# Performance work log

Hardware: AMD Instinct MI355X
Metric: run time of the kernel (lower is better)

## Reference

```python
import jax, jax.numpy as jnp
import numpy as np

N = 100000
E = 1600000
IN_DIM = 128
OUT_DIM = 128
H = 4
HD = OUT_DIM // H  # 32
NEG_SLOPE = 0.2
EPS_SOFTMAX = 1e-8
EPS_LN = 1e-5


def setup_inputs() -> dict:
    key = jax.random.key(0)
    ks = jax.random.split(key, 6)
    h = jax.random.normal(ks[0], (N, IN_DIM), dtype=jnp.float32)
    edge_index = jax.random.randint(ks[1], (2, E), 0, N, dtype=jnp.int32)
    W = jax.random.normal(ks[2], (IN_DIM, OUT_DIM), dtype=jnp.float32) / np.sqrt(IN_DIM)
    W_self = jax.random.normal(ks[3], (IN_DIM, OUT_DIM), dtype=jnp.float32) / np.sqrt(IN_DIM)
    a_in = jax.random.normal(ks[4], (H, 2 * HD), dtype=jnp.float32) * 0.01
    a_out = jax.random.normal(ks[5], (H, 2 * HD), dtype=jnp.float32) * 0.01
    bias = jnp.zeros((OUT_DIM,), dtype=jnp.float32)
    ln_gamma = jnp.ones((OUT_DIM,), dtype=jnp.float32)
    ln_beta = jnp.zeros((OUT_DIM,), dtype=jnp.float32)
    return {"h": h, "edge_index": edge_index, "W": W, "W_self": W_self,
            "a_in": a_in, "a_out": a_out, "bias": bias,
            "ln_gamma": ln_gamma, "ln_beta": ln_beta}


def _attention_aggregate(h_proj, sender, receiver, attn_vec, num_nodes):
    # h_proj: (N, H, HD); sender/receiver: (E,); attn_vec: (H, 2*HD)
    h_sender = h_proj[sender]      # (E, H, HD)
    h_receiver = h_proj[receiver]  # (E, H, HD)
    # e = sum over concat([h_sender, h_receiver]) * attn_vec, split halves
    e = (jnp.einsum('ehd,hd->eh', h_sender, attn_vec[:, :HD])
         + jnp.einsum('ehd,hd->eh', h_receiver, attn_vec[:, HD:]))
    e = jax.nn.leaky_relu(e, NEG_SLOPE)
    e_max = jax.ops.segment_max(e, receiver, num_segments=num_nodes)  # (N, H)
    alpha = jnp.exp(e - e_max[receiver])
    alpha_sum = jax.ops.segment_sum(alpha, receiver, num_segments=num_nodes)
    alpha = alpha / (alpha_sum[receiver] + EPS_SOFTMAX)
    msg = h_sender * alpha[..., None]  # (E, H, HD)
    return jax.ops.segment_sum(msg, receiver, num_segments=num_nodes)  # (N, H, HD)


def reference(h, edge_index, W, W_self, a_in, a_out, bias, ln_gamma, ln_beta):
    n = h.shape[0]
    h_proj = (h @ W).reshape(n, H, HD)
    h_self = h @ W_self
    src, dst = edge_index[0], edge_index[1]
    h_in = _attention_aggregate(h_proj, src, dst, a_in, n)   # 'in' direction
    h_out = _attention_aggregate(h_proj, dst, src, a_out, n)  # 'out' direction
    combined = h_self + h_in.reshape(n, -1) + h_out.reshape(n, -1) + bias
    mean = combined.mean(axis=-1, keepdims=True)
    var = combined.var(axis=-1, keepdims=True)
    normed = (combined - mean) * jax.lax.rsqrt(var + EPS_LN)
    return normed * ln_gamma + ln_beta
```

## Files before the change

### kernel.cpp

```cpp
#include <hip/hip_runtime.h>
#include <math.h>

#define HEADS 4
#define HD 32
#define DIM 128
#define NEG_SLOPE 0.2f
#define EPS_SM 1e-8f
#define EPS_LN 1e-5f
#define SH1 9
#define PB 128
#define BCOLS 272

typedef _Float16 h2_t __attribute__((ext_vector_type(2)));
typedef _Float16 f16x8 __attribute__((ext_vector_type(8)));
typedef float f32x4 __attribute__((ext_vector_type(4)));

__device__ __forceinline__ float lrelu(float x) { return x > 0.f ? x : NEG_SLOPE * x; }
__device__ __forceinline__ unsigned pkh(float a, float b) {
    return __builtin_bit_cast(unsigned, __builtin_amdgcn_cvt_pkrtz(a, b));
}
__device__ __forceinline__ float dot2(unsigned a, unsigned b, float c) {
    return __builtin_amdgcn_fdot2(__builtin_bit_cast(h2_t, a), __builtin_bit_cast(h2_t, b), c, false);
}

template<int LIM> __device__ __forceinline__ void rmax4(float& a, float& b, float& c, float& d) {
#pragma unroll
    for (int s = 1; s < LIM; s <<= 1) {
        a = fmaxf(a, __shfl_xor(a, s, 64));
        b = fmaxf(b, __shfl_xor(b, s, 64));
        c = fmaxf(c, __shfl_xor(c, s, 64));
        d = fmaxf(d, __shfl_xor(d, s, 64));
    }
}
template<int LIM> __device__ __forceinline__ void rsum4(float& a, float& b, float& c, float& d) {
#pragma unroll
    for (int s = 1; s < LIM; s <<= 1) {
        a += __shfl_xor(a, s, 64);
        b += __shfl_xor(b, s, 64);
        c += __shfl_xor(c, s, 64);
        d += __shfl_xor(d, s, 64);
    }
}

__global__ __launch_bounds__(128) void cvtb_k(const float* __restrict__ W,
                                              const float* __restrict__ V,
                                              const float* __restrict__ a_in,
                                              const float* __restrict__ a_out,
                                              _Float16* __restrict__ Bt) {
    const int c = blockIdx.x;
    const int k = threadIdx.x;
    float v;
    if (c < 128) {
        v = W[k * 128 + c];
    } else if (c < 256) {
        v = V[k * 128 + (c - 128)];
    } else {
        int d = (c - 256) >> 2, h = (c - 256) & 3;
        const float* a = (d < 2) ? a_in : a_out;
        int base = h * 64 + (d & 1) * 32;
        float s = 0.f;
#pragma unroll
        for (int t = 0; t < 32; ++t) s += W[k * 128 + 32 * h + t] * a[base + t];
        v = s;
    }
    Bt[c * 128 + k] = (_Float16)v;
}

__global__ __launch_bounds__(256) void mfma_gemm_k(const float* __restrict__ h,
                                                   const _Float16* __restrict__ Bt,
                                                   float* __restrict__ h_self,
                                                   unsigned* __restrict__ hp_pk,
                                                   float* __restrict__ pA0, float* __restrict__ pA1,
                                                   float* __restrict__ pB0, float* __restrict__ pB1,
                                                   int N) {
    __shared__ _Float16 hs[64][128];
    const int tid = threadIdx.x;
    const int w = tid >> 6, l = tid & 63;
    const int l15 = l & 15;
    const int kg = l >> 4;
    const int row0 = blockIdx.x * 64;
    const int arow = row0 + 16 * w + l15;

    f32x4 acc[17];
#pragma unroll
    for (int j = 0; j < 17; ++j) {
        acc[j][0] = 0.f; acc[j][1] = 0.f; acc[j][2] = 0.f; acc[j][3] = 0.f;
    }

    const uint4* __restrict__ bt4 = (const uint4*)Bt;

#pragma unroll
    for (int kc = 0; kc < 4; ++kc) {
        union { unsigned u[4]; f16x8 v; } cv;
        if (arow < N) {
            float4 x0 = ((const float4*)h)[(size_t)arow * 32 + kc * 8 + kg * 2];
            float4 x1 = ((const float4*)h)[(size_t)arow * 32 + kc * 8 + kg * 2 + 1];
            cv.u[0] = pkh(x0.x, x0.y); cv.u[1] = pkh(x0.z, x0.w);
            cv.u[2] = pkh(x1.x, x1.y); cv.u[3] = pkh(x1.z, x1.w);
        } else {
            cv.u[0] = 0u; cv.u[1] = 0u; cv.u[2] = 0u; cv.u[3] = 0u;
        }
        f16x8 af = cv.v;
#pragma unroll
        for (int j = 0; j < 17; ++j) {
            int col = 16 * j + l15;
            union { uint4 q; f16x8 v; } bc;
            bc.q = bt4[col * 16 + kc * 4 + kg];
            acc[j] = __builtin_amdgcn_mfma_f32_16x16x32_f16(af, bc.v, acc[j], 0, 0, 0);
        }
    }

    const int r4 = kg * 4;
    const int c16 = l15, dsel = c16 >> 2, hh = c16 & 3;
    float* __restrict__ pd = (dsel == 0) ? pA0 : (dsel == 1) ? pA1 : (dsel == 2) ? pB0 : pB1;
#pragma unroll
    for (int r = 0; r < 4; ++r) {
        int grow = row0 + 16 * w + r4 + r;
        bool ok = grow < N;
#pragma unroll
        for (int j = 8; j < 16; ++j)
            if (ok) h_self[(size_t)grow * 128 + 16 * (j - 8) + l15] = acc[j][r];
        if (ok) pd[grow * 4 + hh] = acc[16][r];
#pragma unroll
        for (int j = 0; j < 8; ++j)
            hs[16 * w + r4 + r][16 * j + l15] = (_Float16)acc[j][r];
    }
    __syncthreads();
    const uint4* hsv = (const uint4*)&hs[0][0];
#pragma unroll
    for (int p = 0; p < 4; ++p) {
        int chunk = tid + p * 256;
        int rrow = chunk >> 4, cg = chunk & 15;
        int grow = row0 + rrow;
        if (grow < N)
            ((uint4*)hp_pk)[(size_t)grow * 16 + cg] = hsv[rrow * 16 + cg];
    }
}

__global__ __launch_bounds__(256) void part1a_k(const int* __restrict__ ei, int* __restrict__ cntmat,
                                                int E, int N, int NBIN) {
    __shared__ int lcnt[512];
    const int t = threadIdx.x;
    const int CH = (E + gridDim.x - 1) / gridDim.x;
    const int e0 = blockIdx.x * CH;
    const int e1 = min(e0 + CH, E);
    for (int i = t; i < 512; i += 256) lcnt[i] = 0;
    __syncthreads();
    for (int e = e0 + t; e < e1; e += 256) {
        int s = ei[e], d = ei[E + e];
        atomicAdd(&lcnt[d >> SH1], 1);
        atomicAdd(&lcnt[(N + s) >> SH1], 1);
    }
    __syncthreads();
    for (int i = t; i < NBIN; i += 256) cntmat[i * PB + blockIdx.x] = lcnt[i];
}

__global__ __launch_bounds__(128) void scanB_k(const int* __restrict__ cntmat,
                                               int* __restrict__ blkoff, int* __restrict__ btot) {
    __shared__ int ls[PB];
    const int bin = blockIdx.x;
    const int t = threadIdx.x;
    int v = cntmat[bin * PB + t];
    ls[t] = v;
    __syncthreads();
#pragma unroll
    for (int d = 1; d < PB; d <<= 1) {
        int u = (t >= d) ? ls[t - d] : 0;
        __syncthreads();
        ls[t] += u;
        __syncthreads();
    }
    blkoff[bin * PB + t] = ls[t] - v;
    if (t == PB - 1) btot[bin] = ls[t];
}

__global__ __launch_bounds__(256) void scanC_k(const int* __restrict__ btot,
                                               int* __restrict__ bbase, int NBIN, int twoE) {
    __shared__ int ls[256];
    int t = threadIdx.x;
    int i0 = 2 * t, i1 = 2 * t + 1;
    int v0 = (i0 < NBIN) ? btot[i0] : 0;
    int v1 = (i1 < NBIN) ? btot[i1] : 0;
    int pair = v0 + v1;
    ls[t] = pair;
    __syncthreads();
#pragma unroll
    for (int d = 1; d < 256; d <<= 1) {
        int u = (t >= d) ? ls[t - d] : 0;
        __syncthreads();
        ls[t] += u;
        __syncthreads();
    }
    int excl = ls[t] - pair;
    if (i0 < NBIN) bbase[i0] = excl;
    if (i1 < NBIN) bbase[i1] = excl + v0;
    if (t == 0) bbase[NBIN] = twoE;
}

__global__ __launch_bounds__(256) void part1b_k(const int* __restrict__ ei,
                                                const int* __restrict__ bbase,
                                                const int* __restrict__ blkoff,
                                                unsigned* __restrict__ rec, int E, int N, int NBIN) {
    __shared__ int gb[512];
    __shared__ int lcur[512];
    const int t = threadIdx.x;
    const int CH = (E + gridDim.x - 1) / gridDim.x;
    const int e0 = blockIdx.x * CH;
    const int e1 = min(e0 + CH, E);
    for (int i = t; i < 512; i += 256) lcur[i] = 0;
    for (int i = t; i < NBIN; i += 256) gb[i] = bbase[i] + blkoff[i * PB + blockIdx.x];
    __syncthreads();
    for (int e = e0 + t; e < e1; e += 256) {
        int s = ei[e], d = ei[E + e];
        int b1 = d >> SH1;
        int r1 = atomicAdd(&lcur[b1], 1);
        rec[gb[b1] + r1] = (unsigned)s | ((unsigned)(d & 511) << 20);
        int so = N + s;
        int b2 = so >> SH1;
        int r2 = atomicAdd(&lcur[b2], 1);
        rec[gb[b2] + r2] = (unsigned)d | ((unsigned)(so & 511) << 20);
    }
}

__global__ __launch_bounds__(256) void build2_k(const unsigned* __restrict__ rec,
                                                const int* __restrict__ bbase,
                                                int* __restrict__ off, int* __restrict__ csr,
                                                int M, int twoE, int NBIN) {
    __shared__ int lcnt[512];
    __shared__ int lcur[512];
    __shared__ int ls[256];
    const int b = blockIdx.x;
    const int t = threadIdx.x;
    const int base = bbase[b];
    const int cnt = bbase[b + 1] - base;
    const int seg0 = b << SH1;
    for (int i = t; i < 512; i += 256) lcnt[i] = 0;
    __syncthreads();
    for (int k = t; k < cnt; k += 256) atomicAdd(&lcnt[rec[base + k] >> 20], 1);
    __syncthreads();
    int v0 = lcnt[2 * t], v1 = lcnt[2 * t + 1];
    int pair = v0 + v1;
    ls[t] = pair;
    __syncthreads();
#pragma unroll
    for (int d = 1; d < 256; d <<= 1) {
        int u = (t >= d) ? ls[t - d] : 0;
        __syncthreads();
        ls[t] += u;
        __syncthreads();
    }
    int excl = ls[t] - pair;
    lcur[2 * t] = excl;
    lcur[2 * t + 1] = excl + v0;
    int sg = seg0 + 2 * t;
    if (sg < M) off[sg] = base + excl;
    if (sg + 1 < M) off[sg + 1] = base + excl + v0;
    if (b == NBIN - 1 && t == 0) off[M] = twoE;
    __syncthreads();
    for (int k = t; k < cnt; k += 256) {
        unsigned r = rec[base + k];
        int pos = atomicAdd(&lcur[r >> 20], 1);
        csr[base + pos] = (int)(r & 0xFFFFFu);
    }
}

__global__ __launch_bounds__(256) void node_aggr_ln_k(const unsigned* __restrict__ hp_pk,
                                                      const float* __restrict__ h_self,
                                                      const float* __restrict__ pA0, const float* __restrict__ pA1,
                                                      const float* __restrict__ pB0, const float* __restrict__ pB1,
                                                      const int* __restrict__ off, const int* __restrict__ csr,
                                                      const float* __restrict__ bias,
                                                      const float* __restrict__ gamma,
                                                      const float* __restrict__ beta,
                                                      float* __restrict__ out, int N) {
    __shared__ int sds[4][64];
    __shared__ uint2 wts[4][64];
    const int wave = threadIdx.x >> 6;
    const int lane = threadIdx.x & 63;
    const int n = blockIdx.x * 4 + wave;
    if (n >= N) return;
    const int l15 = lane & 15;
    const int q = lane >> 4;
    const unsigned wsel = (l15 & 4) ? 0x07060302u : 0x05040100u;
    const bool hlo = (l15 < 8);
    int* sdw = sds[wave];
    uint2* wtw = wts[wave];
    const char* hpb = (const char*)hp_pk;
    const unsigned rowoff = (unsigned)l15 << 4;

    float acc[8];
#pragma unroll
    for (int k = 0; k < 8; ++k) acc[k] = 0.f;

#pragma unroll
    for (int dir = 0; dir < 2; ++dir) {
        const int seg = (dir == 0) ? n : N + n;
        const int beg = off[seg], end = off[seg + 1];
        const int len = end - beg;
        if (len == 0) continue;
        const float* __restrict__ p0 = (dir == 0) ? pA0 : pB0;
        const float* __restrict__ p1 = (dir == 0) ? pA1 : pB1;
        float4 r1 = ((const float4*)p1)[n];

        if (len <= 64) {
            int sid = 0;
            float e0 = -INFINITY, e1 = -INFINITY, e2 = -INFINITY, e3 = -INFINITY;
            if (lane < len) {
                sid = csr[beg + lane];
                float4 r0 = ((const float4*)p0)[sid];
                e0 = lrelu(r0.x + r1.x);
                e1 = lrelu(r0.y + r1.y);
                e2 = lrelu(r0.z + r1.z);
                e3 = lrelu(r0.w + r1.w);
            }
            float m0 = e0, m1 = e1, m2 = e2, m3 = e3;
            if (len <= 16)      rmax4<16>(m0, m1, m2, m3);
            else if (len <= 32) rmax4<32>(m0, m1, m2, m3);
            else                rmax4<64>(m0, m1, m2, m3);
            float w0 = 0.f, w1 = 0.f, w2 = 0.f, w3 = 0.f;
            if (lane < len) {
                w0 = __expf(e0 - m0); w1 = __expf(e1 - m1);
                w2 = __expf(e2 - m2); w3 = __expf(e3 - m3);
            }
            float s0 = w0, s1 = w1, s2 = w2, s3 = w3;
            if (len <= 16)      rsum4<16>(s0, s1, s2, s3);
            else if (len <= 32) rsum4<32>(s0, s1, s2, s3);
            else                rsum4<64>(s0, s1, s2, s3);
            w0 *= 1.f / (s0 + EPS_SM);
            w1 *= 1.f / (s1 + EPS_SM);
            w2 *= 1.f / (s2 + EPS_SM);
            w3 *= 1.f / (s3 + EPS_SM);
            sdw[lane] = sid;
            wtw[lane] = make_uint2(pkh(w0, w1), pkh(w2, w3));
            const int npair = (len + 7) >> 3;
#pragma unroll 2
            for (int t = 0; t < npair; ++t) {
                int pi = 4 * t + q;
                uint2 sp = *(const uint2*)&sdw[2 * pi];
                uint4 wp = *(const uint4*)&wtw[2 * pi];
                uint4 u = *(const uint4*)(hpb + (((unsigned)sp.x << 8) + rowoff));
                uint4 v = *(const uint4*)(hpb + (((unsigned)sp.y << 8) + rowoff));
                unsigned wA = hlo ? wp.x : wp.y;
                unsigned wB = hlo ? wp.z : wp.w;
                unsigned wpk = __builtin_amdgcn_perm(wB, wA, wsel);
                acc[0] = dot2(__builtin_amdgcn_perm(v.x, u.x, 0x05040100u), wpk, acc[0]);
                acc[1] = dot2(__builtin_amdgcn_perm(v.x, u.x, 0x07060302u), wpk, acc[1]);
                acc[2] = dot2(__builtin_amdgcn_perm(v.y, u.y, 0x05040100u), wpk, acc[2]);
                acc[3] = dot2(__builtin_amdgcn_perm(v.y, u.y, 0x07060302u), wpk, acc[3]);
                acc[4] = dot2(__builtin_amdgcn_perm(v.z, u.z, 0x05040100u), wpk, acc[4]);
                acc[5] = dot2(__builtin_amdgcn_perm(v.z, u.z, 0x07060302u), wpk, acc[5]);
                acc[6] = dot2(__builtin_amdgcn_perm(v.w, u.w, 0x05040100u), wpk, acc[6]);
                acc[7] = dot2(__builtin_amdgcn_perm(v.w, u.w, 0x07060302u), wpk, acc[7]);
            }
        } else {
            float m0 = -INFINITY, m1 = -INFINITY, m2 = -INFINITY, m3 = -INFINITY;
            for (int base = beg; base < end; base += 64) {
                int j = base + lane;
                if (j < end) {
                    int sid = csr[j];
                    float4 r0 = ((const float4*)p0)[sid];
                    m0 = fmaxf(m0, lrelu(r0.x + r1.x));
                    m1 = fmaxf(m1, lrelu(r0.y + r1.y));
                    m2 = fmaxf(m2, lrelu(r0.z + r1.z));
                    m3 = fmaxf(m3, lrelu(r0.w + r1.w));
                }
            }
            rmax4<64>(m0, m1, m2, m3);
            float s0 = 0.f, s1 = 0.f, s2 = 0.f, s3 = 0.f;
            for (int base = beg; base < end; base += 64) {
                int j = base + lane;
                if (j < end) {
                    int sid = csr[j];
                    float4 r0 = ((const float4*)p0)[sid];
                    s0 += __expf(lrelu(r0.x + r1.x) - m0);
                    s1 += __expf(lrelu(r0.y + r1.y) - m1);
                    s2 += __expf(lrelu(r0.z + r1.z) - m2);
                    s3 += __expf(lrelu(r0.w + r1.w) - m3);
                }
            }
            rsum4<64>(s0, s1, s2, s3);
            const float is0 = 1.f / (s0 + EPS_SM);
            const float is1 = 1.f / (s1 + EPS_SM);
            const float is2 = 1.f / (s2 + EPS_SM);
            const float is3 = 1.f / (s3 + EPS_SM);
            for (int base = beg; base < end; base += 64) {
                int cnt = min(64, end - base);
                int sid = 0;
                float w0 = 0.f, w1 = 0.f, w2 = 0.f, w3 = 0.f;
                if (lane < cnt) {
                    sid = csr[base + lane];
                    float4 r0 = ((const float4*)p0)[sid];
                    w0 = __expf(lrelu(r0.x + r1.x) - m0) * is0;
                    w1 = __expf(lrelu(r0.y + r1.y) - m1) * is1;
                    w2 = __expf(lrelu(r0.z + r1.z) - m2) * is2;
                    w3 = __expf(lrelu(r0.w + r1.w) - m3) * is3;
                }
                sdw[lane] = sid;
                wtw[lane] = make_uint2(pkh(w0, w1), pkh(w2, w3));
                const int npair = (cnt + 7) >> 3;
#pragma unroll 2
                for (int t = 0; t < npair; ++t) {
                    int pi = 4 * t + q;
                    uint2 sp = *(const uint2*)&sdw[2 * pi];
                    uint4 wp = *(const uint4*)&wtw[2 * pi];
                    uint4 u = *(const uint4*)(hpb + (((unsigned)sp.x << 8) + rowoff));
                    uint4 v = *(const uint4*)(hpb + (((unsigned)sp.y << 8) + rowoff));
                    unsigned wA = hlo ? wp.x : wp.y;
                    unsigned wB = hlo ? wp.z : wp.w;
                    unsigned wpk = __builtin_amdgcn_perm(wB, wA, wsel);
                    acc[0] = dot2(__builtin_amdgcn_perm(v.x, u.x, 0x05040100u), wpk, acc[0]);
                    acc[1] = dot2(__builtin_amdgcn_perm(v.x, u.x, 0x07060302u), wpk, acc[1]);
                    acc[2] = dot2(__builtin_amdgcn_perm(v.y, u.y, 0x05040100u), wpk, acc[2]);
                    acc[3] = dot2(__builtin_amdgcn_perm(v.y, u.y, 0x07060302u), wpk, acc[3]);
                    acc[4] = dot2(__builtin_amdgcn_perm(v.z, u.z, 0x05040100u), wpk, acc[4]);
                    acc[5] = dot2(__builtin_amdgcn_perm(v.z, u.z, 0x07060302u), wpk, acc[5]);
                    acc[6] = dot2(__builtin_amdgcn_perm(v.w, u.w, 0x05040100u), wpk, acc[6]);
                    acc[7] = dot2(__builtin_amdgcn_perm(v.w, u.w, 0x07060302u), wpk, acc[7]);
                }
            }
        }
    }

#pragma unroll
    for (int s = 16; s < 64; s <<= 1) {
#pragma unroll
        for (int k = 0; k < 8; ++k) acc[k] += __shfl_xor(acc[k], s, 64);
    }

    size_t bb = (size_t)n * DIM;
    float4 hs0 = ((const float4*)(h_self + bb))[2 * l15];
    float4 hs1 = ((const float4*)(h_self + bb))[2 * l15 + 1];
    float4 b0 = ((const float4*)bias)[2 * l15];
    float4 b1 = ((const float4*)bias)[2 * l15 + 1];
    float x0 = hs0.x + acc[0] + b0.x;
    float x1 = hs0.y + acc[1] + b0.y;
    float x2 = hs0.z + acc[2] + b0.z;
    float x3 = hs0.w + acc[3] + b0.w;
    float y0 = hs1.x + acc[4] + b1.x;
    float y1 = hs1.y + acc[5] + b1.y;
    float y2 = hs1.z + acc[6] + b1.z;
    float y3 = hs1.w + acc[7] + b1.w;
    float sum = x0 + x1 + x2 + x3 + y0 + y1 + y2 + y3;
    float sq = x0 * x0 + x1 * x1 + x2 * x2 + x3 * x3
             + y0 * y0 + y1 * y1 + y2 * y2 + y3 * y3;
#pragma unroll
    for (int m = 1; m < 64; m <<= 1) {
        sum += __shfl_xor(sum, m, 64);
        sq += __shfl_xor(sq, m, 64);
    }
    float mean = sum * (1.f / 512.f);
    float var = sq * (1.f / 512.f) - mean * mean;
    float inv = rsqrtf(var + EPS_LN);
    if (lane < 16) {
        float4 g0 = ((const float4*)gamma)[2 * l15];
        float4 g1 = ((const float4*)gamma)[2 * l15 + 1];
        float4 be0 = ((const float4*)beta)[2 * l15];
        float4 be1 = ((const float4*)beta)[2 * l15 + 1];
        float4 o0 = make_float4((x0 - mean) * inv * g0.x + be0.x,
                                (x1 - mean) * inv * g0.y + be0.y,
                                (x2 - mean) * inv * g0.z + be0.z,
                                (x3 - mean) * inv * g0.w + be0.w);
        float4 o1 = make_float4((y0 - mean) * inv * g1.x + be1.x,
                                (y1 - mean) * inv * g1.y + be1.y,
                                (y2 - mean) * inv * g1.z + be1.z,
                                (y3 - mean) * inv * g1.w + be1.w);
        ((float4*)(out + bb))[2 * l15] = o0;
        ((float4*)(out + bb))[2 * l15 + 1] = o1;
    }
}

extern "C" void kernel_launch(void* const* d_in, const int* in_sizes, int n_in,
                              void* d_out, int out_size, void* d_ws, size_t ws_size,
                              hipStream_t stream) {
    const float* h      = (const float*)d_in[0];
    const int*   ei     = (const int*)d_in[1];
    const float* W      = (const float*)d_in[2];
    const float* W_self = (const float*)d_in[3];
    const float* a_in   = (const float*)d_in[4];
    const float* a_out  = (const float*)d_in[5];
    const float* bias   = (const float*)d_in[6];
    const float* gamma  = (const float*)d_in[7];
    const float* beta   = (const float*)d_in[8];
    float* out = (float*)d_out;

    const int N = in_sizes[0] / DIM;
    const int E = in_sizes[1] / 2;
    const int M = 2 * N;
    const int NBIN = (M + (1 << SH1) - 1) >> SH1;
    const int twoE = 2 * E;

    float* ws = (float*)d_ws;
    size_t off_f = 0;
    float* h_self = ws + off_f; off_f += (size_t)N * DIM;
    unsigned* hp_pk = (unsigned*)(ws + off_f); off_f += (size_t)N * 64;
    float* pA0 = ws + off_f; off_f += (size_t)N * 4;
    float* pA1 = ws + off_f; off_f += (size_t)N * 4;
    float* pB0 = ws + off_f; off_f += (size_t)N * 4;
    float* pB1 = ws + off_f; off_f += (size_t)N * 4;
    int* ip = (int*)(ws + off_f);
    size_t off_i = 0;
    int* cntmat = ip + off_i; off_i += (size_t)NBIN * PB;
    int* blkoff = ip + off_i; off_i += (size_t)NBIN * PB;
    int* btot   = ip + off_i; off_i += NBIN;
    int* bbase  = ip + off_i; off_i += (size_t)NBIN + 1;
    int* off    = ip + off_i; off_i += (size_t)M + 1;
    unsigned* rec = (unsigned*)(ip + off_i); off_i += (size_t)twoE;
    int* csr    = ip + off_i; off_i += (size_t)twoE;
    _Float16* Bt = (_Float16*)(ip + off_i); off_i += (size_t)(BCOLS * 128) / 2;

    cvtb_k<<<BCOLS, 128, 0, stream>>>(W, W_self, a_in, a_out, Bt);

    part1a_k<<<PB, 256, 0, stream>>>(ei, cntmat, E, N, NBIN);
    scanB_k<<<NBIN, PB, 0, stream>>>(cntmat, blkoff, btot);
    scanC_k<<<1, 256, 0, stream>>>(btot, bbase, NBIN, twoE);
    part1b_k<<<PB, 256, 0, stream>>>(ei, bbase, blkoff, rec, E, N, NBIN);
    build2_k<<<NBIN, 256, 0, stream>>>(rec, bbase, off, csr, M, twoE, NBIN);

    mfma_gemm_k<<<(N + 63) / 64, 256, 0, stream>>>(h, Bt, h_self, hp_pk,
                                                   pA0, pA1, pB0, pB1, N);

    node_aggr_ln_k<<<(N + 3) / 4, 256, 0, stream>>>(hp_pk, h_self, pA0, pA1, pB0, pB1,
                                                    off, csr, bias, gamma, beta, out, N);
}
```

Baseline: 417.1 us.

## Fuse weight prep into count kernel, store h_self in fp16, merge both directions

Folds the weight-conversion kernel into the edge-count kernel as extra blocks, removing one launch. Stores the self-projection h_self as packed fp16 instead of fp32, halving its write and read traffic. Processes both edge directions in one pass over the wave when each degree is at most 32, with each half-wave handling one direction and a shared aggregation loop. The fp16 h_self costs some precision in the residual term.

```diff
diff --git a/kernel.cpp b/kernel.cpp
--- a/kernel.cpp
+++ b/kernel.cpp
@@ -22,6 +22,8 @@
 __device__ __forceinline__ float dot2(unsigned a, unsigned b, float c) {
     return __builtin_amdgcn_fdot2(__builtin_bit_cast(h2_t, a), __builtin_bit_cast(h2_t, b), c, false);
 }
+__device__ __forceinline__ float lo16(unsigned u) { return (float)__builtin_bit_cast(h2_t, u)[0]; }
+__device__ __forceinline__ float hi16(unsigned u) { return (float)__builtin_bit_cast(h2_t, u)[1]; }
 
 template<int LIM> __device__ __forceinline__ void rmax4(float& a, float& b, float& c, float& d) {
 #pragma unroll
@@ -42,38 +44,85 @@
     }
 }
 
-__global__ __launch_bounds__(128) void cvtb_k(const float* __restrict__ W,
-                                              const float* __restrict__ V,
-                                              const float* __restrict__ a_in,
-                                              const float* __restrict__ a_out,
-                                              _Float16* __restrict__ Bt) {
-    const int c = blockIdx.x;
-    const int k = threadIdx.x;
-    float v;
-    if (c < 128) {
-        v = W[k * 128 + c];
-    } else if (c < 256) {
-        v = V[k * 128 + (c - 128)];
-    } else {
-        int d = (c - 256) >> 2, h = (c - 256) & 3;
-        const float* a = (d < 2) ? a_in : a_out;
-        int base = h * 64 + (d & 1) * 32;
-        float s = 0.f;
-#pragma unroll
-        for (int t = 0; t < 32; ++t) s += W[k * 128 + 32 * h + t] * a[base + t];
-        v = s;
-    }
-    Bt[c * 128 + k] = (_Float16)v;
+__device__ __forceinline__ void aggr_pairs(int cnt, const int* __restrict__ sdw,
+                                           const uint2* __restrict__ wtw,
+                                           const char* __restrict__ hpb,
+                                           unsigned rowoff, int q, bool hlo, unsigned wsel,
+                                           float (&acc)[8]) {
+    const int npair = (cnt + 7) >> 3;
+#pragma unroll 2
+    for (int t = 0; t < npair; ++t) {
+        int pi = 4 * t + q;
+        uint2 sp = *(const uint2*)&sdw[2 * pi];
+        uint4 wp = *(const uint4*)&wtw[2 * pi];
+        uint4 u = *(const uint4*)(hpb + (((unsigned)sp.x << 8) + rowoff));
+        uint4 v = *(const uint4*)(hpb + (((unsigned)sp.y << 8) + rowoff));
+        unsigned wA = hlo ? wp.x : wp.y;
+        unsigned wB = hlo ? wp.z : wp.w;
+        unsigned wpk = __builtin_amdgcn_perm(wB, wA, wsel);
+        acc[0] = dot2(__builtin_amdgcn_perm(v.x, u.x, 0x05040100u), wpk, acc[0]);
+        acc[1] = dot2(__builtin_amdgcn_perm(v.x, u.x, 0x07060302u), wpk, acc[1]);
+        acc[2] = dot2(__builtin_amdgcn_perm(v.y, u.y, 0x05040100u), wpk, acc[2]);
+        acc[3] = dot2(__builtin_amdgcn_perm(v.y, u.y, 0x07060302u), wpk, acc[3]);
+        acc[4] = dot2(__builtin_amdgcn_perm(v.z, u.z, 0x05040100u), wpk, acc[4]);
+        acc[5] = dot2(__builtin_amdgcn_perm(v.z, u.z, 0x07060302u), wpk, acc[5]);
+        acc[6] = dot2(__builtin_amdgcn_perm(v.w, u.w, 0x05040100u), wpk, acc[6]);
+        acc[7] = dot2(__builtin_amdgcn_perm(v.w, u.w, 0x07060302u), wpk, acc[7]);
+    }
+}
+
+__global__ __launch_bounds__(256) void part1a_k(const int* __restrict__ ei, int* __restrict__ cntmat,
+                                                int E, int N, int NBIN,
+                                                const float* __restrict__ W,
+                                                const float* __restrict__ V,
+                                                const float* __restrict__ a_in,
+                                                const float* __restrict__ a_out,
+                                                _Float16* __restrict__ Bt) {
+    __shared__ int lcnt[512];
+    const int t = threadIdx.x;
+    if (blockIdx.x >= PB) {
+        int c = (blockIdx.x - PB) * 2 + (t >> 7);
+        int k = t & 127;
+        float v;
+        if (c < 128) {
+            v = W[k * 128 + c];
+        } else if (c < 256) {
+            v = V[k * 128 + (c - 128)];
+        } else {
+            int d = (c - 256) >> 2, hh = (c - 256) & 3;
+            const float* a = (d < 2) ? a_in : a_out;
+            int base = hh * 64 + (d & 1) * 32;
+            float s = 0.f;
+#pragma unroll
+            for (int tt = 0; tt < 32; ++tt) s += W[k * 128 + 32 * hh + tt] * a[base + tt];
+            v = s;
+        }
+        Bt[c * 128 + k] = (_Float16)v;
+        return;
+    }
+    const int CH = (E + PB - 1) / PB;
+    const int e0 = blockIdx.x * CH;
+    const int e1 = min(e0 + CH, E);
+    for (int i = t; i < 512; i += 256) lcnt[i] = 0;
+    __syncthreads();
+    for (int e = e0 + t; e < e1; e += 256) {
+        int s = ei[e], d = ei[E + e];
+        atomicAdd(&lcnt[d >> SH1], 1);
+        atomicAdd(&lcnt[(N + s) >> SH1], 1);
+    }
+    __syncthreads();
+    for (int i = t; i < NBIN; i += 256) cntmat[i * PB + blockIdx.x] = lcnt[i];
 }
 
 __global__ __launch_bounds__(256) void mfma_gemm_k(const float* __restrict__ h,
                                                    const _Float16* __restrict__ Bt,
-                                                   float* __restrict__ h_self,
+                                                   unsigned* __restrict__ hs_pk,
                                                    unsigned* __restrict__ hp_pk,
                                                    float* __restrict__ pA0, float* __restrict__ pA1,
                                                    float* __restrict__ pB0, float* __restrict__ pB1,
                                                    int N) {
     __shared__ _Float16 hs[64][128];
+    __shared__ _Float16 hss[64][128];
     const int tid = threadIdx.x;
     const int w = tid >> 6, l = tid & 63;
     const int l15 = l & 15;
@@ -111,48 +160,33 @@
     }
 
     const int r4 = kg * 4;
-    const int c16 = l15, dsel = c16 >> 2, hh = c16 & 3;
+    const int dsel = l15 >> 2, hh = l15 & 3;
     float* __restrict__ pd = (dsel == 0) ? pA0 : (dsel == 1) ? pA1 : (dsel == 2) ? pB0 : pB1;
 #pragma unroll
     for (int r = 0; r < 4; ++r) {
-        int grow = row0 + 16 * w + r4 + r;
-        bool ok = grow < N;
+        int lr = 16 * w + r4 + r;
+        int grow = row0 + lr;
+#pragma unroll
+        for (int j = 0; j < 8; ++j)
+            hs[lr][16 * j + l15] = (_Float16)acc[j][r];
 #pragma unroll
         for (int j = 8; j < 16; ++j)
-            if (ok) h_self[(size_t)grow * 128 + 16 * (j - 8) + l15] = acc[j][r];
-        if (ok) pd[grow * 4 + hh] = acc[16][r];
-#pragma unroll
-        for (int j = 0; j < 8; ++j)
-            hs[16 * w + r4 + r][16 * j + l15] = (_Float16)acc[j][r];
+            hss[lr][16 * (j - 8) + l15] = (_Float16)acc[j][r];
+        if (grow < N) pd[grow * 4 + hh] = acc[16][r];
     }
     __syncthreads();
     const uint4* hsv = (const uint4*)&hs[0][0];
+    const uint4* hssv = (const uint4*)&hss[0][0];
 #pragma unroll
     for (int p = 0; p < 4; ++p) {
         int chunk = tid + p * 256;
         int rrow = chunk >> 4, cg = chunk & 15;
         int grow = row0 + rrow;
-        if (grow < N)
+        if (grow < N) {
             ((uint4*)hp_pk)[(size_t)grow * 16 + cg] = hsv[rrow * 16 + cg];
-    }
-}
-
-__global__ __launch_bounds__(256) void part1a_k(const int* __restrict__ ei, int* __restrict__ cntmat,
-                                                int E, int N, int NBIN) {
-    __shared__ int lcnt[512];
-    const int t = threadIdx.x;
-    const int CH = (E + gridDim.x - 1) / gridDim.x;
-    const int e0 = blockIdx.x * CH;
-    const int e1 = min(e0 + CH, E);
-    for (int i = t; i < 512; i += 256) lcnt[i] = 0;
-    __syncthreads();
-    for (int e = e0 + t; e < e1; e += 256) {
-        int s = ei[e], d = ei[E + e];
-        atomicAdd(&lcnt[d >> SH1], 1);
-        atomicAdd(&lcnt[(N + s) >> SH1], 1);
-    }
-    __syncthreads();
-    for (int i = t; i < NBIN; i += 256) cntmat[i * PB + blockIdx.x] = lcnt[i];
+            ((uint4*)hs_pk)[(size_t)grow * 16 + cg] = hssv[rrow * 16 + cg];
+        }
+    }
 }
 
 __global__ __launch_bounds__(128) void scanB_k(const int* __restrict__ cntmat,
@@ -265,7 +299,7 @@
 }
 
 __global__ __launch_bounds__(256) void node_aggr_ln_k(const unsigned* __restrict__ hp_pk,
-                                                      const float* __restrict__ h_self,
+                                                      const unsigned* __restrict__ hs_pk,
                                                       const float* __restrict__ pA0, const float* __restrict__ pA1,
                                                       const float* __restrict__ pB0, const float* __restrict__ pB1,
                                                       const int* __restrict__ off, const int* __restrict__ csr,
@@ -292,132 +326,138 @@
 #pragma unroll
     for (int k = 0; k < 8; ++k) acc[k] = 0.f;
 
-#pragma unroll
-    for (int dir = 0; dir < 2; ++dir) {
-        const int seg = (dir == 0) ? n : N + n;
-        const int beg = off[seg], end = off[seg + 1];
-        const int len = end - beg;
-        if (len == 0) continue;
-        const float* __restrict__ p0 = (dir == 0) ? pA0 : pB0;
-        const float* __restrict__ p1 = (dir == 0) ? pA1 : pB1;
-        float4 r1 = ((const float4*)p1)[n];
-
-        if (len <= 64) {
-            int sid = 0;
-            float e0 = -INFINITY, e1 = -INFINITY, e2 = -INFINITY, e3 = -INFINITY;
-            if (lane < len) {
-                sid = csr[beg + lane];
-                float4 r0 = ((const float4*)p0)[sid];
-                e0 = lrelu(r0.x + r1.x);
-                e1 = lrelu(r0.y + r1.y);
-                e2 = lrelu(r0.z + r1.z);
-                e3 = lrelu(r0.w + r1.w);
-            }
-            float m0 = e0, m1 = e1, m2 = e2, m3 = e3;
-            if (len <= 16)      rmax4<16>(m0, m1, m2, m3);
-            else if (len <= 32) rmax4<32>(m0, m1, m2, m3);
-            else                rmax4<64>(m0, m1, m2, m3);
-            float w0 = 0.f, w1 = 0.f, w2 = 0.f, w3 = 0.f;
-            if (lane < len) {
-                w0 = __expf(e0 - m0); w1 = __expf(e1 - m1);
-                w2 = __expf(e2 - m2); w3 = __expf(e3 - m3);
-            }
-            float s0 = w0, s1 = w1, s2 = w2, s3 = w3;
-            if (len <= 16)      rsum4<16>(s0, s1, s2, s3);
-            else if (len <= 32) rsum4<32>(s0, s1, s2, s3);
-            else                rsum4<64>(s0, s1, s2, s3);
-            w0 *= 1.f / (s0 + EPS_SM);
-            w1 *= 1.f / (s1 + EPS_SM);
-            w2 *= 1.f / (s2 + EPS_SM);
-            w3 *= 1.f / (s3 + EPS_SM);
-            sdw[lane] = sid;
-            wtw[lane] = make_uint2(pkh(w0, w1), pkh(w2, w3));
-            const int npair = (len + 7) >> 3;
-#pragma unroll 2
-            for (int t = 0; t < npair; ++t) {
-                int pi = 4 * t + q;
-                uint2 sp = *(const uint2*)&sdw[2 * pi];
-                uint4 wp = *(const uint4*)&wtw[2 * pi];
-                uint4 u = *(const uint4*)(hpb + (((unsigned)sp.x << 8) + rowoff));
-                uint4 v = *(const uint4*)(hpb + (((unsigned)sp.y << 8) + rowoff));
-                unsigned wA = hlo ? wp.x : wp.y;
-                unsigned wB = hlo ? wp.z : wp.w;
-                unsigned wpk = __builtin_amdgcn_perm(wB, wA, wsel);
-                acc[0] = dot2(__builtin_amdgcn_perm(v.x, u.x, 0x05040100u), wpk, acc[0]);
-                acc[1] = dot2(__builtin_amdgcn_perm(v.x, u.x, 0x07060302u), wpk, acc[1]);
-                acc[2] = dot2(__builtin_amdgcn_perm(v.y, u.y, 0x05040100u), wpk, acc[2]);
-                acc[3] = dot2(__builtin_amdgcn_perm(v.y, u.y, 0x07060302u), wpk, acc[3]);
-                acc[4] = dot2(__builtin_amdgcn_perm(v.z, u.z, 0x05040100u), wpk, acc[4]);
-                acc[5] = dot2(__builtin_amdgcn_perm(v.z, u.z, 0x07060302u), wpk, acc[5]);
-                acc[6] = dot2(__builtin_amdgcn_perm(v.w, u.w, 0x05040100u), wpk, acc[6]);
-                acc[7] = dot2(__builtin_amdgcn_perm(v.w, u.w, 0x07060302u), wpk, acc[7]);
-            }
-        } else {
-            float m0 = -INFINITY, m1 = -INFINITY, m2 = -INFINITY, m3 = -INFINITY;
-            for (int base = beg; base < end; base += 64) {
-                int j = base + lane;
-                if (j < end) {
-                    int sid = csr[j];
+    const int beg0 = off[n], end0 = off[n + 1];
+    const int beg1 = off[N + n], end1 = off[N + n + 1];
+    const int len0 = end0 - beg0, len1 = end1 - beg1;
+
+    if (len0 <= 32 && len1 <= 32) {
+        const int half = lane >> 5;
+        const int hl = lane & 31;
+        const int beg = half ? beg1 : beg0;
+        const int len = half ? len1 : len0;
+        const float* __restrict__ pp0 = half ? pB0 : pA0;
+        const float* __restrict__ pp1 = half ? pB1 : pA1;
+        float4 r1 = ((const float4*)pp1)[n];
+        int sid = 0;
+        float e0 = -INFINITY, e1 = -INFINITY, e2 = -INFINITY, e3 = -INFINITY;
+        if (hl < len) {
+            sid = csr[beg + hl];
+            float4 r0 = ((const float4*)pp0)[sid];
+            e0 = lrelu(r0.x + r1.x);
+            e1 = lrelu(r0.y + r1.y);
+            e2 = lrelu(r0.z + r1.z);
+            e3 = lrelu(r0.w + r1.w);
+        }
+        float m0 = e0, m1 = e1, m2 = e2, m3 = e3;
+        const bool small16 = (len0 <= 16 && len1 <= 16);
+        if (small16) rmax4<16>(m0, m1, m2, m3);
+        else         rmax4<32>(m0, m1, m2, m3);
+        float w0 = 0.f, w1 = 0.f, w2 = 0.f, w3 = 0.f;
+        if (hl < len) {
+            w0 = __expf(e0 - m0); w1 = __expf(e1 - m1);
+            w2 = __expf(e2 - m2); w3 = __expf(e3 - m3);
+        }
+        float s0 = w0, s1 = w1, s2 = w2, s3 = w3;
+        if (small16) rsum4<16>(s0, s1, s2, s3);
+        else         rsum4<32>(s0, s1, s2, s3);
+        w0 *= 1.f / (s0 + EPS_SM);
+        w1 *= 1.f / (s1 + EPS_SM);
+        w2 *= 1.f / (s2 + EPS_SM);
+        w3 *= 1.f / (s3 + EPS_SM);
+        sdw[lane] = 0;
+        wtw[lane] = make_uint2(0u, 0u);
+        if (hl < len) {
+            int pos = half ? len0 + hl : hl;
+            sdw[pos] = sid;
+            wtw[pos] = make_uint2(pkh(w0, w1), pkh(w2, w3));
+        }
+        aggr_pairs(len0 + len1, sdw, wtw, hpb, rowoff, q, hlo, wsel, acc);
+    } else {
+#pragma unroll
+        for (int dir = 0; dir < 2; ++dir) {
+            const int beg = (dir == 0) ? beg0 : beg1;
+            const int end = (dir == 0) ? end0 : end1;
+            const int len = end - beg;
+            if (len == 0) continue;
+            const float* __restrict__ p0 = (dir == 0) ? pA0 : pB0;
+            const float* __restrict__ p1 = (dir == 0) ? pA1 : pB1;
+            float4 r1 = ((const float4*)p1)[n];
+
+            if (len <= 64) {
+                int sid = 0;
+                float e0 = -INFINITY, e1 = -INFINITY, e2 = -INFINITY, e3 = -INFINITY;
+                if (lane < len) {
+                    sid = csr[beg + lane];
                     float4 r0 = ((const float4*)p0)[sid];
-                    m0 = fmaxf(m0, lrelu(r0.x + r1.x));
-                    m1 = fmaxf(m1, lrelu(r0.y + r1.y));
-                    m2 = fmaxf(m2, lrelu(r0.z + r1.z));
-                    m3 = fmaxf(m3, lrelu(r0.w + r1.w));
+                    e0 = lrelu(r0.x + r1.x);
+                    e1 = lrelu(r0.y + r1.y);
+                    e2 = lrelu(r0.z + r1.z);
+                    e3 = lrelu(r0.w + r1.w);
+                }
+                float m0 = e0, m1 = e1, m2 = e2, m3 = e3;
+                rmax4<64>(m0, m1, m2, m3);
+                float w0 = 0.f, w1 = 0.f, w2 = 0.f, w3 = 0.f;
+                if (lane < len) {
+                    w0 = __expf(e0 - m0); w1 = __expf(e1 - m1);
+                    w2 = __expf(e2 - m2); w3 = __expf(e3 - m3);
+                }
+                float s0 = w0, s1 = w1, s2 = w2, s3 = w3;
+                rsum4<64>(s0, s1, s2, s3);
+                w0 *= 1.f / (s0 + EPS_SM);
+                w1 *= 1.f / (s1 + EPS_SM);
+                w2 *= 1.f / (s2 + EPS_SM);
+                w3 *= 1.f / (s3 + EPS_SM);
+                sdw[lane] = sid;
+                wtw[lane] = make_uint2(pkh(w0, w1), pkh(w2, w3));
+                aggr_pairs(len, sdw, wtw, hpb, rowoff, q, hlo, wsel, acc);
+            } else {
+                float m0 = -INFINITY, m1 = -INFINITY, m2 = -INFINITY, m3 = -INFINITY;
+                for (int base = beg; base < end; base += 64) {
+                    int j = base + lane;
+                    if (j < end) {
+                        int sid = csr[j];
+                        float4 r0 = ((const float4*)p0)[sid];
+                        m0 = fmaxf(m0, lrelu(r0.x + r1.x));
+                        m1 = fmaxf(m1, lrelu(r0.y + r1.y));
+                        m2 = fmaxf(m2, lrelu(r0.z + r1.z));
+                        m3 = fmaxf(m3, lrelu(r0.w + r1.w));
+                    }
+                }
+                rmax4<64>(m0, m1, m2, m3);
+                float s0 = 0.f, s1 = 0.f, s2 = 0.f, s3 = 0.f;
+                for (int base = beg; base < end; base += 64) {
+                    int j = base + lane;
+                    if (j < end) {
+                        int sid = csr[j];
+                        float4 r0 = ((const float4*)p0)[sid];
+                        s0 += __expf(lrelu(r0.x + r1.x) - m0);
+                        s1 += __expf(lrelu(r0.y + r1.y) - m1);
+                        s2 += __expf(lrelu(r0.z + r1.z) - m2);
+                        s3 += __expf(lrelu(r0.w + r1.w) - m3);
+                    }
+                }
+                rsum4<64>(s0, s1, s2, s3);
+                const float is0 = 1.f / (s0 + EPS_SM);
+                const float is1 = 1.f / (s1 + EPS_SM);
+                const float is2 = 1.f / (s2 + EPS_SM);
+                const float is3 = 1.f / (s3 + EPS_SM);
+                for (int base = beg; base < end; base += 64) {
+                    int cnt = min(64, end - base);
+                    int sid = 0;
+                    float w0 = 0.f, w1 = 0.f, w2 = 0.f, w3 = 0.f;
+                    if (lane < cnt) {
+                        sid = csr[base + lane];
+                        float4 r0 = ((const float4*)p0)[sid];
+                        w0 = __expf(lrelu(r0.x + r1.x) - m0) * is0;
+                        w1 = __expf(lrelu(r0.y + r1.y) - m1) * is1;
+                        w2 = __expf(lrelu(r0.z + r1.z) - m2) * is2;
+                        w3 = __expf(lrelu(r0.w + r1.w) - m3) * is3;
+                    }
+                    sdw[lane] = sid;
+                    wtw[lane] = make_uint2(pkh(w0, w1), pkh(w2, w3));
+                    aggr_pairs(cnt, sdw, wtw, hpb, rowoff, q, hlo, wsel, acc);
                 }
             }
-            rmax4<64>(m0, m1, m2, m3);
-            float s0 = 0.f, s1 = 0.f, s2 = 0.f, s3 = 0.f;
-            for (int base = beg; base < end; base += 64) {
-                int j = base + lane;
-                if (j < end) {
-                    int sid = csr[j];
-                    float4 r0 = ((const float4*)p0)[sid];
-                    s0 += __expf(lrelu(r0.x + r1.x) - m0);
-                    s1 += __expf(lrelu(r0.y + r1.y) - m1);
-                    s2 += __expf(lrelu(r0.z + r1.z) - m2);
-                    s3 += __expf(lrelu(r0.w + r1.w) - m3);
-                }
-            }
-            rsum4<64>(s0, s1, s2, s3);
-            const float is0 = 1.f / (s0 + EPS_SM);
-            const float is1 = 1.f / (s1 + EPS_SM);
-            const float is2 = 1.f / (s2 + EPS_SM);
-            const float is3 = 1.f / (s3 + EPS_SM);
-            for (int base = beg; base < end; base += 64) {
-                int cnt = min(64, end - base);
-                int sid = 0;
-                float w0 = 0.f, w1 = 0.f, w2 = 0.f, w3 = 0.f;
-                if (lane < cnt) {
-                    sid = csr[base + lane];
-                    float4 r0 = ((const float4*)p0)[sid];
-                    w0 = __expf(lrelu(r0.x + r1.x) - m0) * is0;
-                    w1 = __expf(lrelu(r0.y + r1.y) - m1) * is1;
-                    w2 = __expf(lrelu(r0.z + r1.z) - m2) * is2;
-                    w3 = __expf(lrelu(r0.w + r1.w) - m3) * is3;
-                }
-                sdw[lane] = sid;
-                wtw[lane] = make_uint2(pkh(w0, w1), pkh(w2, w3));
-                const int npair = (cnt + 7) >> 3;
-#pragma unroll 2
-                for (int t = 0; t < npair; ++t) {
-                    int pi = 4 * t + q;
-                    uint2 sp = *(const uint2*)&sdw[2 * pi];
-                    uint4 wp = *(const uint4*)&wtw[2 * pi];
-                    uint4 u = *(const uint4*)(hpb + (((unsigned)sp.x << 8) + rowoff));
-                    uint4 v = *(const uint4*)(hpb + (((unsigned)sp.y << 8) + rowoff));
-                    unsigned wA = hlo ? wp.x : wp.y;
-                    unsigned wB = hlo ? wp.z : wp.w;
-                    unsigned wpk = __builtin_amdgcn_perm(wB, wA, wsel);
-                    acc[0] = dot2(__builtin_amdgcn_perm(v.x, u.x, 0x05040100u), wpk, acc[0]);
-                    acc[1] = dot2(__builtin_amdgcn_perm(v.x, u.x, 0x07060302u), wpk, acc[1]);
-                    acc[2] = dot2(__builtin_amdgcn_perm(v.y, u.y, 0x05040100u), wpk, acc[2]);
-                    acc[3] = dot2(__builtin_amdgcn_perm(v.y, u.y, 0x07060302u), wpk, acc[3]);
-                    acc[4] = dot2(__builtin_amdgcn_perm(v.z, u.z, 0x05040100u), wpk, acc[4]);
-                    acc[5] = dot2(__builtin_amdgcn_perm(v.z, u.z, 0x07060302u), wpk, acc[5]);
-                    acc[6] = dot2(__builtin_amdgcn_perm(v.w, u.w, 0x05040100u), wpk, acc[6]);
-                    acc[7] = dot2(__builtin_amdgcn_perm(v.w, u.w, 0x07060302u), wpk, acc[7]);
-                }
-            }
         }
     }
 
@@ -428,18 +468,17 @@
     }
 
     size_t bb = (size_t)n * DIM;
-    float4 hs0 = ((const float4*)(h_self + bb))[2 * l15];
-    float4 hs1 = ((const float4*)(h_self + bb))[2 * l15 + 1];
+    uint4 hv = ((const uint4*)hs_pk)[(size_t)n * 16 + l15];
     float4 b0 = ((const float4*)bias)[2 * l15];
     float4 b1 = ((const float4*)bias)[2 * l15 + 1];
-    float x0 = hs0.x + acc[0] + b0.x;
-    float x1 = hs0.y + acc[1] + b0.y;
-    float x2 = hs0.z + acc[2] + b0.z;
-    float x3 = hs0.w + acc[3] + b0.w;
-    float y0 = hs1.x + acc[4] + b1.x;
-    float y1 = hs1.y + acc[5] + b1.y;
-    float y2 = hs1.z + acc[6] + b1.z;
-    float y3 = hs1.w + acc[7] + b1.w;
+    float x0 = lo16(hv.x) + acc[0] + b0.x;
+    float x1 = hi16(hv.x) + acc[1] + b0.y;
+    float x2 = lo16(hv.y) + acc[2] + b0.z;
+    float x3 = hi16(hv.y) + acc[3] + b0.w;
+    float y0 = lo16(hv.z) + acc[4] + b1.x;
+    float y1 = hi16(hv.z) + acc[5] + b1.y;
+    float y2 = lo16(hv.w) + acc[6] + b1.z;
+    float y3 = hi16(hv.w) + acc[7] + b1.w;
     float sum = x0 + x1 + x2 + x3 + y0 + y1 + y2 + y3;
     float sq = x0 * x0 + x1 * x1 + x2 * x2 + x3 * x3
              + y0 * y0 + y1 * y1 + y2 * y2 + y3 * y3;
@@ -491,7 +530,7 @@
 
     float* ws = (float*)d_ws;
     size_t off_f = 0;
-    float* h_self = ws + off_f; off_f += (size_t)N * DIM;
+    unsigned* hs_pk = (unsigned*)(ws + off_f); off_f += (size_t)N * 64;
     unsigned* hp_pk = (unsigned*)(ws + off_f); off_f += (size_t)N * 64;
     float* pA0 = ws + off_f; off_f += (size_t)N * 4;
     float* pA1 = ws + off_f; off_f += (size_t)N * 4;
@@ -508,17 +547,16 @@
     int* csr    = ip + off_i; off_i += (size_t)twoE;
     _Float16* Bt = (_Float16*)(ip + off_i); off_i += (size_t)(BCOLS * 128) / 2;
 
-    cvtb_k<<<BCOLS, 128, 0, stream>>>(W, W_self, a_in, a_out, Bt);
-
-    part1a_k<<<PB, 256, 0, stream>>>(ei, cntmat, E, N, NBIN);
+    part1a_k<<<PB + BCOLS / 2, 256, 0, stream>>>(ei, cntmat, E, N, NBIN,
+                                                 W, W_self, a_in, a_out, Bt);
     scanB_k<<<NBIN, PB, 0, stream>>>(cntmat, blkoff, btot);
     scanC_k<<<1, 256, 0, stream>>>(btot, bbase, NBIN, twoE);
     part1b_k<<<PB, 256, 0, stream>>>(ei, bbase, blkoff, rec, E, N, NBIN);
     build2_k<<<NBIN, 256, 0, stream>>>(rec, bbase, off, csr, M, twoE, NBIN);
 
-    mfma_gemm_k<<<(N + 63) / 64, 256, 0, stream>>>(h, Bt, h_self, hp_pk,
+    mfma_gemm_k<<<(N + 63) / 64, 256, 0, stream>>>(h, Bt, hs_pk, hp_pk,
                                                    pA0, pA1, pB0, pB1, N);
 
-    node_aggr_ln_k<<<(N + 3) / 4, 256, 0, stream>>>(hp_pk, h_self, pA0, pA1, pB0, pB1,
+    node_aggr_ln_k<<<(N + 3) / 4, 256, 0, stream>>>(hp_pk, hs_pk, pA0, pA1, pB0, pB1,
                                                     off, csr, bias, gamma, beta, out, N);
 }
```

Measured after the change: 398.1 us. -4.5%, faster.
